# Kernel tuning notes

Hardware: AMD Instinct MI355X
Metric: run time of the kernel (lower is better)

## Reference

```python
import jax, jax.numpy as jnp
import numpy as np

DIM = 1024
RANK = 16


def setup_inputs() -> dict:
    key = jax.random.key(0)
    ks = jax.random.split(key, 9)
    s = 0.02
    return {
        "x": jax.random.normal(ks[0], (2, 4096, DIM), dtype=jnp.float32),
        "W_qkv": jax.random.normal(ks[1], (3 * DIM, DIM), dtype=jnp.float32) * s,
        "b_qkv": jax.random.normal(ks[2], (3 * DIM,), dtype=jnp.float32) * s,
        "A_q": jax.random.normal(ks[3], (RANK, DIM), dtype=jnp.float32) * s,
        "B_q": jax.random.normal(ks[4], (DIM, RANK), dtype=jnp.float32) * s,
        "A_k": jax.random.normal(ks[5], (RANK, DIM), dtype=jnp.float32) * s,
        "B_k": jax.random.normal(ks[6], (DIM, RANK), dtype=jnp.float32) * s,
        "A_v": jax.random.normal(ks[7], (RANK, DIM), dtype=jnp.float32) * s,
        "B_v": jax.random.normal(ks[8], (DIM, RANK), dtype=jnp.float32) * s,
        "alpha": jnp.float32(0.5),
    }


def reference(x, W_qkv, b_qkv, A_q, B_q, A_k, B_k, A_v, B_v, alpha):
    # base fused QKV projection: [B, S, 3*dim]
    qkv = jnp.einsum("bsd,od->bso", x, W_qkv) + b_qkv
    # low-rank adapters: x @ A.T @ B.T, rank=16
    lora_q = jnp.einsum("bsr,dr->bsd", jnp.einsum("bsd,rd->bsr", x, A_q), B_q)
    lora_k = jnp.einsum("bsr,dr->bsd", jnp.einsum("bsd,rd->bsr", x, A_k), B_k)
    lora_v = jnp.einsum("bsr,dr->bsd", jnp.einsum("bsd,rd->bsr", x, A_v), B_v)
    # scaled add into q/k/v slices (concat order matches torch slice layout)
    delta = jnp.concatenate([lora_q, lora_k, lora_v], axis=-1)
    return qkv + alpha * delta
```

## Files before the change

kernel.cpp:

```cpp
#include <hip/hip_runtime.h>
#include <stdint.h>

#define DIM    1024
#define RANK   16
#define M_TOT  8192
#define N_TOT  3072
#define K_TOT  1024

#define BM 256
#define BN 128
#define BK 64
#define NT (K_TOT / BK)

typedef __attribute__((ext_vector_type(8))) short  s8v;
typedef __attribute__((ext_vector_type(4))) float  f4v;

__device__ __forceinline__ unsigned short f2bf(float f) {
    union { float f; unsigned int u; } v; v.f = f;
    unsigned int u = v.u;
    u += 0x7FFFu + ((u >> 16) & 1u);
    return (unsigned short)(u >> 16);
}

__device__ __forceinline__ void gload_lds16(const unsigned short* g,
                                            unsigned short* l) {
    __builtin_amdgcn_global_load_lds(
        (const __attribute__((address_space(1))) void*)g,
        (__attribute__((address_space(3))) void*)l,
        16, 0, 0);
}

__global__ void prep(const float4* __restrict__ x, ushort4* __restrict__ xb,
                     const float* __restrict__ W,
                     const float* __restrict__ Aq, const float* __restrict__ Bq,
                     const float* __restrict__ Ak, const float* __restrict__ Bk,
                     const float* __restrict__ Av, const float* __restrict__ Bv,
                     const float* __restrict__ alpha_p,
                     unsigned short* __restrict__ Wb) {
    const int tid = threadIdx.x;
    if (blockIdx.x < 8192) {
        int i = blockIdx.x * 256 + tid;
        float4 v = x[i];
        ushort4 o;
        o.x = f2bf(v.x); o.y = f2bf(v.y); o.z = f2bf(v.z); o.w = f2bf(v.w);
        xb[i] = o;
    } else {
        const int o    = blockIdx.x - 8192;
        const int sel  = o >> 10;
        const int orow = o & 1023;
        const float* Am = (sel == 0) ? Aq : (sel == 1) ? Ak : Av;
        const float* Bm = (sel == 0) ? Bq : (sel == 1) ? Bk : Bv;

        __shared__ float sb[RANK];
        if (tid < RANK) sb[tid] = alpha_p[0] * Bm[orow * RANK + tid];
        __syncthreads();

        for (int d = tid; d < DIM; d += 256) {
            float acc = W[o * DIM + d];
            #pragma unroll
            for (int r = 0; r < RANK; ++r)
                acc += sb[r] * Am[r * DIM + d];
            Wb[o * DIM + d] = f2bf(acc);
        }
    }
}

__global__ __launch_bounds__(512, 2)
void gemm_bt(const unsigned short* __restrict__ Xb,
             const unsigned short* __restrict__ Wb,
             const float* __restrict__ bias,
             float* __restrict__ out) {
    __shared__ __align__(16) unsigned short As[2][BM * BK];
    __shared__ __align__(16) unsigned short Bs[2][BN * BK];

    const int tid  = threadIdx.x;
    const int wave = tid >> 6;
    const int lane = tid & 63;
    const int l15  = lane & 15;
    const int lq   = lane >> 4;
    const int wr   = wave >> 1;
    const int wc   = wave & 1;

    const int bid  = blockIdx.x;
    const int wgid = (bid & 7) * 96 + (bid >> 3);
    const int bn   = wgid >> 5;
    const int bm   = wgid & 31;

    const unsigned short* aptr[4];
    const unsigned short* bptr[2];
    int aoff[4], boff[2];
    #pragma unroll
    for (int u = 0; u < 4; ++u) {
        const int c   = wave * 4 + u;
        const int row = ((c >> 1) << 4) + l15;
        const int col = ((c & 1) << 5) + (lq << 3);
        aptr[u] = Xb + (size_t)(bm * BM + row) * K_TOT + col;
        aoff[u] = c * 512;
    }
    #pragma unroll
    for (int u = 0; u < 2; ++u) {
        const int c   = wave * 2 + u;
        const int row = ((c >> 1) << 4) + l15;
        const int col = ((c & 1) << 5) + (lq << 3);
        bptr[u] = Wb + (size_t)(bn * BN + row) * K_TOT + col;
        boff[u] = c * 512;
    }

    #pragma unroll
    for (int t = 0; t < 2; ++t) {
        #pragma unroll
        for (int u = 0; u < 4; ++u) gload_lds16(aptr[u] + t * BK, &As[t][aoff[u]]);
        #pragma unroll
        for (int u = 0; u < 2; ++u) gload_lds16(bptr[u] + t * BK, &Bs[t][boff[u]]);
    }

    f4v acc[4][4] = {};

    #pragma unroll
    for (int kt = 0; kt < NT; ++kt) {
        const int cur = kt & 1;
        if (kt < NT - 1) asm volatile("s_waitcnt vmcnt(6)" ::: "memory");
        else             asm volatile("s_waitcnt vmcnt(0)" ::: "memory");
        __builtin_amdgcn_sched_barrier(0);
        __builtin_amdgcn_s_barrier();
        __builtin_amdgcn_sched_barrier(0);
        asm volatile("" ::: "memory");

        const s8v* Avp = (const s8v*)As[cur];
        const s8v* Bvp = (const s8v*)Bs[cur];
        #pragma unroll
        for (int t = 0; t < 2; ++t) {
            s8v af[4], bf[4];
            #pragma unroll
            for (int i = 0; i < 4; ++i) {
                af[i] = Avp[((wr * 4 + i) * 2 + t) * 64 + lane];
                bf[i] = Bvp[((wc * 4 + i) * 2 + t) * 64 + lane];
            }
            #pragma unroll
            for (int i = 0; i < 4; ++i)
                #pragma unroll
                for (int j = 0; j < 4; ++j)
                    acc[i][j] = __builtin_amdgcn_mfma_f32_16x16x32_bf16(
                        af[i], bf[j], acc[i][j], 0, 0, 0);
        }

        asm volatile("" ::: "memory");
        __builtin_amdgcn_sched_barrier(0);
        __builtin_amdgcn_s_barrier();
        __builtin_amdgcn_sched_barrier(0);

        if (kt < NT - 2) {
            #pragma unroll
            for (int u = 0; u < 4; ++u)
                gload_lds16(aptr[u] + (kt + 2) * BK, &As[cur][aoff[u]]);
            #pragma unroll
            for (int u = 0; u < 2; ++u)
                gload_lds16(bptr[u] + (kt + 2) * BK, &Bs[cur][boff[u]]);
        }
    }

    const int col_base = bn * BN + wc * 64;
    const int row_base = bm * BM + wr * 64 + lq * 4;
    #pragma unroll
    for (int j = 0; j < 4; ++j) {
        const int col = col_base + j * 16 + l15;
        const float bv = bias[col];
        #pragma unroll
        for (int i = 0; i < 4; ++i) {
            const int row = row_base + i * 16;
            #pragma unroll
            for (int r = 0; r < 4; ++r)
                out[(size_t)(row + r) * N_TOT + col] = acc[i][j][r] + bv;
        }
    }
}

extern "C" void kernel_launch(void* const* d_in, const int* in_sizes, int n_in,
                              void* d_out, int out_size, void* d_ws, size_t ws_size,
                              hipStream_t stream) {
    const float* x     = (const float*)d_in[0];
    const float* W     = (const float*)d_in[1];
    const float* b     = (const float*)d_in[2];
    const float* Aq    = (const float*)d_in[3];
    const float* Bq    = (const float*)d_in[4];
    const float* Ak    = (const float*)d_in[5];
    const float* Bk    = (const float*)d_in[6];
    const float* Av    = (const float*)d_in[7];
    const float* Bv    = (const float*)d_in[8];
    const float* alpha = (const float*)d_in[9];
    float* out = (float*)d_out;

    unsigned short* xb = (unsigned short*)d_ws;
    unsigned short* Wb = (unsigned short*)((char*)d_ws + (size_t)M_TOT * K_TOT * 2);

    prep<<<8192 + N_TOT, 256, 0, stream>>>((const float4*)x, (ushort4*)xb,
                                           W, Aq, Bq, Ak, Bk, Av, Bv, alpha, Wb);

    gemm_bt<<<(M_TOT / BM) * (N_TOT / BN), 512, 0, stream>>>(xb, Wb, b, out);
}
```

Before: 261.0 us.

## Restructure prep kernel, remap GEMM tiles per XCD, peel K-loop tail

The prep kernel now converts four float4 chunks of x per thread and folds the LoRA delta into W in 16-row blocks, with A rows held in registers, so A is read once per block instead of once per output row and far fewer blocks are launched. The GEMM block-to-tile mapping changes so each XCD owns a contiguous band of M tiles across all N tiles, aiming for better L2 reuse of X. The K loop drops its per-iteration branches by peeling the last two iterations and unrolling by two. The tradeoffs are higher register pressure in prep (16 float4 A values per thread) and larger code size in the GEMM.

```diff
diff --git a/kernel.cpp b/kernel.cpp
--- a/kernel.cpp
+++ b/kernel.cpp
@@ -30,37 +30,57 @@
         16, 0, 0);
 }
 
-__global__ void prep(const float4* __restrict__ x, ushort4* __restrict__ xb,
-                     const float* __restrict__ W,
-                     const float* __restrict__ Aq, const float* __restrict__ Bq,
-                     const float* __restrict__ Ak, const float* __restrict__ Bk,
-                     const float* __restrict__ Av, const float* __restrict__ Bv,
-                     const float* __restrict__ alpha_p,
-                     unsigned short* __restrict__ Wb) {
+__global__ __launch_bounds__(256)
+void prep(const float4* __restrict__ x, ushort4* __restrict__ xb,
+          const float* __restrict__ W,
+          const float* __restrict__ Aq, const float* __restrict__ Bq,
+          const float* __restrict__ Ak, const float* __restrict__ Bk,
+          const float* __restrict__ Av, const float* __restrict__ Bv,
+          const float* __restrict__ alpha_p,
+          unsigned short* __restrict__ Wb) {
     const int tid = threadIdx.x;
-    if (blockIdx.x < 8192) {
+    if (blockIdx.x < 2048) {
         int i = blockIdx.x * 256 + tid;
-        float4 v = x[i];
-        ushort4 o;
-        o.x = f2bf(v.x); o.y = f2bf(v.y); o.z = f2bf(v.z); o.w = f2bf(v.w);
-        xb[i] = o;
+        #pragma unroll
+        for (int k = 0; k < 4; ++k) {
+            float4 v = x[i];
+            ushort4 o;
+            o.x = f2bf(v.x); o.y = f2bf(v.y); o.z = f2bf(v.z); o.w = f2bf(v.w);
+            xb[i] = o;
+            i += 2048 * 256;
+        }
     } else {
-        const int o    = blockIdx.x - 8192;
-        const int sel  = o >> 10;
-        const int orow = o & 1023;
+        const int bid2 = blockIdx.x - 2048;
+        const int sel  = bid2 >> 6;
+        const int rb   = bid2 & 63;
         const float* Am = (sel == 0) ? Aq : (sel == 1) ? Ak : Av;
         const float* Bm = (sel == 0) ? Bq : (sel == 1) ? Bk : Bv;
 
-        __shared__ float sb[RANK];
-        if (tid < RANK) sb[tid] = alpha_p[0] * Bm[orow * RANK + tid];
+        __shared__ float sb[16][RANK];
+        {
+            const int row = rb * 16 + (tid >> 4);
+            sb[tid >> 4][tid & 15] = alpha_p[0] * Bm[row * RANK + (tid & 15)];
+        }
         __syncthreads();
 
-        for (int d = tid; d < DIM; d += 256) {
-            float acc = W[o * DIM + d];
+        float4 a4[RANK];
+        #pragma unroll
+        for (int r = 0; r < RANK; ++r)
+            a4[r] = ((const float4*)(Am + r * DIM))[tid];
+
+        #pragma unroll
+        for (int row = 0; row < 16; ++row) {
+            const int o = sel * 1024 + rb * 16 + row;
+            float4 w = ((const float4*)(W + (size_t)o * DIM))[tid];
             #pragma unroll
-            for (int r = 0; r < RANK; ++r)
-                acc += sb[r] * Am[r * DIM + d];
-            Wb[o * DIM + d] = f2bf(acc);
+            for (int r = 0; r < RANK; ++r) {
+                const float s = sb[row][r];
+                w.x += s * a4[r].x; w.y += s * a4[r].y;
+                w.z += s * a4[r].z; w.w += s * a4[r].w;
+            }
+            ushort4 ov;
+            ov.x = f2bf(w.x); ov.y = f2bf(w.y); ov.z = f2bf(w.z); ov.w = f2bf(w.w);
+            ((ushort4*)(Wb + (size_t)o * DIM))[tid] = ov;
         }
     }
 }
@@ -81,10 +101,11 @@
     const int wr   = wave >> 1;
     const int wc   = wave & 1;
 
-    const int bid  = blockIdx.x;
-    const int wgid = (bid & 7) * 96 + (bid >> 3);
-    const int bn   = wgid >> 5;
-    const int bm   = wgid & 31;
+    const int bid = blockIdx.x;
+    const int xcd = bid & 7;
+    const int s   = bid >> 3;
+    const int bn  = s % 24;
+    const int bm  = xcd * 4 + s / 24;
 
     const unsigned short* aptr[4];
     const unsigned short* bptr[2];
@@ -116,48 +137,61 @@
 
     f4v acc[4][4] = {};
 
-    #pragma unroll
-    for (int kt = 0; kt < NT; ++kt) {
+    #define COMPUTE(curbuf)                                                      \
+    {                                                                            \
+        const s8v* Avp = (const s8v*)As[curbuf];                                 \
+        const s8v* Bvp = (const s8v*)Bs[curbuf];                                 \
+        _Pragma("unroll")                                                        \
+        for (int t = 0; t < 2; ++t) {                                            \
+            s8v af[4], bf[4];                                                    \
+            _Pragma("unroll")                                                    \
+            for (int i = 0; i < 4; ++i) {                                        \
+                af[i] = Avp[((wr * 4 + i) * 2 + t) * 64 + lane];                 \
+                bf[i] = Bvp[((wc * 4 + i) * 2 + t) * 64 + lane];                 \
+            }                                                                    \
+            _Pragma("unroll")                                                    \
+            for (int i = 0; i < 4; ++i)                                          \
+                _Pragma("unroll")                                                \
+                for (int j = 0; j < 4; ++j)                                      \
+                    acc[i][j] = __builtin_amdgcn_mfma_f32_16x16x32_bf16(         \
+                        af[i], bf[j], acc[i][j], 0, 0, 0);                       \
+        }                                                                        \
+    }
+
+    #pragma unroll 2
+    for (int kt = 0; kt < NT - 2; ++kt) {
         const int cur = kt & 1;
-        if (kt < NT - 1) asm volatile("s_waitcnt vmcnt(6)" ::: "memory");
-        else             asm volatile("s_waitcnt vmcnt(0)" ::: "memory");
+        asm volatile("s_waitcnt vmcnt(6)" ::: "memory");
         __builtin_amdgcn_sched_barrier(0);
         __builtin_amdgcn_s_barrier();
         __builtin_amdgcn_sched_barrier(0);
-        asm volatile("" ::: "memory");
-
-        const s8v* Avp = (const s8v*)As[cur];
-        const s8v* Bvp = (const s8v*)Bs[cur];
-        #pragma unroll
-        for (int t = 0; t < 2; ++t) {
-            s8v af[4], bf[4];
-            #pragma unroll
-            for (int i = 0; i < 4; ++i) {
-                af[i] = Avp[((wr * 4 + i) * 2 + t) * 64 + lane];
-                bf[i] = Bvp[((wc * 4 + i) * 2 + t) * 64 + lane];
-            }
-            #pragma unroll
-            for (int i = 0; i < 4; ++i)
-                #pragma unroll
-                for (int j = 0; j < 4; ++j)
-                    acc[i][j] = __builtin_amdgcn_mfma_f32_16x16x32_bf16(
-                        af[i], bf[j], acc[i][j], 0, 0, 0);
-        }
-
-        asm volatile("" ::: "memory");
+
+        COMPUTE(cur);
+
         __builtin_amdgcn_sched_barrier(0);
         __builtin_amdgcn_s_barrier();
         __builtin_amdgcn_sched_barrier(0);
 
-        if (kt < NT - 2) {
-            #pragma unroll
-            for (int u = 0; u < 4; ++u)
-                gload_lds16(aptr[u] + (kt + 2) * BK, &As[cur][aoff[u]]);
-            #pragma unroll
-            for (int u = 0; u < 2; ++u)
-                gload_lds16(bptr[u] + (kt + 2) * BK, &Bs[cur][boff[u]]);
-        }
-    }
+        #pragma unroll
+        for (int u = 0; u < 4; ++u)
+            gload_lds16(aptr[u] + (kt + 2) * BK, &As[cur][aoff[u]]);
+        #pragma unroll
+        for (int u = 0; u < 2; ++u)
+            gload_lds16(bptr[u] + (kt + 2) * BK, &Bs[cur][boff[u]]);
+    }
+
+    asm volatile("s_waitcnt vmcnt(6)" ::: "memory");
+    __builtin_amdgcn_sched_barrier(0);
+    __builtin_amdgcn_s_barrier();
+    __builtin_amdgcn_sched_barrier(0);
+    COMPUTE(0);
+
+    asm volatile("s_waitcnt vmcnt(0)" ::: "memory");
+    __builtin_amdgcn_sched_barrier(0);
+    __builtin_amdgcn_s_barrier();
+    __builtin_amdgcn_sched_barrier(0);
+    COMPUTE(1);
+    #undef COMPUTE
 
     const int col_base = bn * BN + wc * 64;
     const int row_base = bm * BM + wr * 64 + lq * 4;
@@ -193,8 +227,8 @@
     unsigned short* xb = (unsigned short*)d_ws;
     unsigned short* Wb = (unsigned short*)((char*)d_ws + (size_t)M_TOT * K_TOT * 2);
 
-    prep<<<8192 + N_TOT, 256, 0, stream>>>((const float4*)x, (ushort4*)xb,
-                                           W, Aq, Bq, Ak, Bk, Av, Bv, alpha, Wb);
+    prep<<<2048 + 192, 256, 0, stream>>>((const float4*)x, (ushort4*)xb,
+                                         W, Aq, Bq, Ak, Bk, Av, Bv, alpha, Wb);
 
     gemm_bt<<<(M_TOT / BM) * (N_TOT / BN), 512, 0, stream>>>(xb, Wb, b, out);
 }
```

Measured after the change: 254.0 us. 2.7% less time.
